# Optimization experiments

Measured on AMD Instinct MI355X. Metric: run time of the kernel, lower is better.

The kernel has to match this reference:

```python
import jax, jax.numpy as jnp
import numpy as np

NEG_INF = -1000000000.0
INPUT_SIZE = 1024
HIDDEN_SIZE = 64
B, S = 8, 2048


def setup_inputs() -> dict:
    key = jax.random.key(0)
    ks = jax.random.split(key, 8)
    scale = 1.0 / np.sqrt(INPUT_SIZE)
    inp = {
        "input": jax.random.normal(ks[0], (B, S, INPUT_SIZE), dtype=jnp.float32),
        "mask": jax.random.randint(ks[1], (B, S, S), 0, 2, dtype=jnp.int32),
        "W_q": jax.random.uniform(ks[2], (HIDDEN_SIZE, INPUT_SIZE), jnp.float32, -scale, scale),
        "b_q": jax.random.uniform(ks[3], (HIDDEN_SIZE,), jnp.float32, -scale, scale),
        "W_k": jax.random.uniform(ks[4], (HIDDEN_SIZE, INPUT_SIZE), jnp.float32, -scale, scale),
        "b_k": jax.random.uniform(ks[5], (HIDDEN_SIZE,), jnp.float32, -scale, scale),
        "W_v": jax.random.uniform(ks[6], (HIDDEN_SIZE, INPUT_SIZE), jnp.float32, -scale, scale),
        "b_v": jax.random.uniform(ks[7], (HIDDEN_SIZE,), jnp.float32, -scale, scale),
    }
    return inp


def reference(input, mask, W_q, b_q, W_k, b_k, W_v, b_v):
    inv_sqrt_d = 1.0 / np.sqrt(HIDDEN_SIZE)
    # Q/K/V projections: torch Linear is x @ W.T + b
    q = jnp.einsum('bsi,hi->bsh', input, W_q) + b_q  # (B,S,H)
    k = jnp.einsum('bsi,hi->bsh', input, W_k) + b_k
    v = jnp.einsum('bsi,hi->bsh', input, W_v) + b_v
    scores = jnp.einsum('bqh,bkh->bqk', q, k) * inv_sqrt_d  # (B,S,S)
    scores = jnp.where(mask == 0, NEG_INF, scores)
    probs = jax.nn.softmax(scores, axis=-1)
    return jnp.einsum('bqk,bkh->bqh', probs, v)  # (B,S,H)
```

## Files before the change

### kernel.cpp

```cpp
#include <hip/hip_runtime.h>

typedef __bf16 bf16;
typedef bf16 bf16x4 __attribute__((ext_vector_type(4)));
typedef bf16 bf16x8 __attribute__((ext_vector_type(8)));
typedef float floatx4 __attribute__((ext_vector_type(4)));
typedef unsigned int u32;

#define B_ 8
#define S_ 2048
#define I_ 1024
#define H_ 64
#define NEG_INF_ -1000000000.0f

__device__ __forceinline__ void async_cp16(bf16* lds_base, const bf16* g_base, int lane) {
    __builtin_amdgcn_global_load_lds(
        (const __attribute__((address_space(1))) u32*)(g_base + lane * 8),
        (__attribute__((address_space(3))) u32*)lds_base, 16, 0, 0);
}

__global__ void conv_w(const float* __restrict__ Wq, const float* __restrict__ bq,
                       const float* __restrict__ Wk, const float* __restrict__ bk,
                       const float* __restrict__ Wv, const float* __restrict__ bv,
                       bf16* __restrict__ Wc2, float* __restrict__ bc) {
    int idx = blockIdx.x * 256 + threadIdx.x;
    int n = idx >> 10, i = idx & 1023;
    float v;
    if (n < 64)       v = Wq[n * I_ + i] * 0.125f;
    else if (n < 128) v = Wk[(n - 64) * I_ + i];
    else              v = Wv[(n - 128) * I_ + i];
    int s = i >> 7, kl = i & 127;
    Wc2[(size_t)s * 26112 + n * 136 + kl] = (bf16)v;
    if (idx < 192) {
        float bb = (idx < 64) ? bq[idx] * 0.125f
                 : (idx < 128) ? bk[idx - 64] : bv[idx - 128];
        bc[idx] = bb;
    }
}

__global__ __launch_bounds__(256, 2) void qkv_gemm(const float* __restrict__ X,
                                                   const bf16* __restrict__ Wc2,
                                                   const float* __restrict__ bc,
                                                   bf16* __restrict__ Qd,
                                                   bf16* __restrict__ Kd2,
                                                   bf16* __restrict__ Vt2) {
    __shared__ __align__(16) bf16 Xs[32 * 136];
    __shared__ __align__(16) bf16 Ws[26112];

    int tid = threadIdx.x;
    int w = tid >> 6, lane = tid & 63;
    int n = lane & 15, g = lane >> 4;
    int m0 = blockIdx.x * 32;
    int mt = w & 1, nh = (w >> 1) * 96;

    floatx4 zero4 = {0.0f, 0.0f, 0.0f, 0.0f};
    floatx4 acc[6];
#pragma unroll
    for (int t = 0; t < 6; ++t) acc[t] = zero4;

    int xrow = tid >> 3, xcb = (tid & 7) * 16;
    const float* xsrc = X + (size_t)(m0 + xrow) * I_ + xcb;
    bf16* xdst = Xs + xrow * 136 + xcb;

    for (int s = 0; s < 8; ++s) {
        const float* xp = xsrc + s * 128;
        float4 x0 = *(const float4*)(xp);
        float4 x1 = *(const float4*)(xp + 4);
        float4 x2 = *(const float4*)(xp + 8);
        float4 x3 = *(const float4*)(xp + 12);
#pragma unroll
        for (int i = 0; i < 13; ++i) {
            int inst = i * 4 + w;
            if (inst < 51)
                async_cp16(Ws + inst * 512, Wc2 + (size_t)s * 26112 + inst * 512, lane);
        }
        bf16x8 b0, b1;
        b0[0] = (bf16)x0.x; b0[1] = (bf16)x0.y; b0[2] = (bf16)x0.z; b0[3] = (bf16)x0.w;
        b0[4] = (bf16)x1.x; b0[5] = (bf16)x1.y; b0[6] = (bf16)x1.z; b0[7] = (bf16)x1.w;
        b1[0] = (bf16)x2.x; b1[1] = (bf16)x2.y; b1[2] = (bf16)x2.z; b1[3] = (bf16)x2.w;
        b1[4] = (bf16)x3.x; b1[5] = (bf16)x3.y; b1[6] = (bf16)x3.z; b1[7] = (bf16)x3.w;
        *(bf16x8*)xdst = b0;
        *(bf16x8*)(xdst + 8) = b1;
        __syncthreads();

#pragma unroll
        for (int ks = 0; ks < 4; ++ks) {
            bf16x8 xa = *(bf16x8*)(Xs + (mt * 16 + n) * 136 + ks * 32 + g * 8);
#pragma unroll
            for (int nt = 0; nt < 6; ++nt) {
                bf16x8 wb = *(bf16x8*)(Ws + (nh + nt * 16 + n) * 136 + ks * 32 + g * 8);
                acc[nt] = __builtin_amdgcn_mfma_f32_16x16x32_bf16(xa, wb, acc[nt], 0, 0, 0);
            }
        }
        __syncthreads();
    }

    int b = m0 >> 11;
    int sb = (m0 & 2047) + mt * 16 + g * 4;
#pragma unroll
    for (int nt = 0; nt < 6; ++nt) {
        int ng = nh + nt * 16 + n;
        float bias = bc[ng];
        if (ng < 64) {
#pragma unroll
            for (int r = 0; r < 4; ++r)
                Qd[(size_t)(b * S_ + sb + r) * H_ + ng] = (bf16)(acc[nt][r] + bias);
        } else if (ng < 128) {
            int hc = (ng - 64) >> 3, j = (ng - 64) & 7;
#pragma unroll
            for (int r = 0; r < 4; ++r)
                Kd2[((size_t)(b * 8 + hc) * S_ + sb + r) * 8 + j] = (bf16)(acc[nt][r] + bias);
        } else {
            int hh = ng - 128, kc = sb >> 3, jj = sb & 7;
            bf16x4 pk;
#pragma unroll
            for (int r = 0; r < 4; ++r) pk[r] = (bf16)(acc[nt][r] + bias);
            *(bf16x4*)(Vt2 + ((size_t)(b * 256 + kc) * 64 + hh) * 8 + jj) = pk;
        }
    }
}

__global__ __launch_bounds__(256, 4) void attn(const bf16* __restrict__ Qd,
                                               const bf16* __restrict__ Kd2,
                                               const bf16* __restrict__ Vt2,
                                               const int* __restrict__ mask,
                                               float* __restrict__ po,
                                               float* __restrict__ pml) {
    __shared__ __align__(16) bf16 regA[8704];
    __shared__ __align__(16) bf16 Vs[16 * 528];

    int tid = threadIdx.x;
    int w = tid >> 6, lane = tid & 63;
    int n = lane & 15, g = lane >> 4;
    int bid = blockIdx.x;
    int ksp = bid & 3;
    int qt = (bid >> 2) & 31;
    int b = bid >> 7;
    int q0 = qt * 64;

    const bf16* qptr = Qd + (size_t)(b * S_ + q0 + w * 16 + n) * H_ + g * 8;
    bf16x8 qa0 = *(const bf16x8*)qptr;
    bf16x8 qa1 = *(const bf16x8*)(qptr + 32);

    floatx4 zero4 = {0.0f, 0.0f, 0.0f, 0.0f};
    floatx4 o[4];
#pragma unroll
    for (int t = 0; t < 4; ++t) o[t] = zero4;
    float m_i[4], l_i[4];
#pragma unroll
    for (int r = 0; r < 4; ++r) { m_i[r] = -INFINITY; l_i[r] = 0.0f; }

    for (int kt = ksp * 4; kt < ksp * 4 + 4; ++kt) {
        const int* mb = mask + (size_t)(b * S_ + q0 + w * 16 + g * 4) * S_ + kt * 128 + n;
        int mreg[4][8];
#pragma unroll
        for (int r = 0; r < 4; ++r)
#pragma unroll
            for (int nt = 0; nt < 8; ++nt)
                mreg[r][nt] = mb[(size_t)r * S_ + nt * 16];
#pragma unroll
        for (int j = 0; j < 4; ++j) {
            int hc = w * 2 + (j >> 1), p = j & 1;
            async_cp16(regA + hc * 1040 + p * 512,
                       Kd2 + ((size_t)(b * 8 + hc) * S_ + kt * 128 + p * 64) * 8, lane);
        }
#pragma unroll
        for (int j = 0; j < 4; ++j) {
            int kcl = w * 4 + j;
            async_cp16(Vs + kcl * 528,
                       Vt2 + ((size_t)(b * 256 + kt * 16 + kcl) * 64) * 8, lane);
        }
        __syncthreads();

        floatx4 s[8];
#pragma unroll
        for (int nt = 0; nt < 8; ++nt) {
            floatx4 a = zero4;
            a = __builtin_amdgcn_mfma_f32_16x16x32_bf16(
                    qa0, *(const bf16x8*)(regA + g * 1040 + (nt * 16 + n) * 8), a, 0, 0, 0);
            a = __builtin_amdgcn_mfma_f32_16x16x32_bf16(
                    qa1, *(const bf16x8*)(regA + (4 + g) * 1040 + (nt * 16 + n) * 8), a, 0, 0, 0);
            s[nt] = a;
        }

#pragma unroll
        for (int r = 0; r < 4; ++r)
#pragma unroll
            for (int nt = 0; nt < 8; ++nt)
                if (mreg[r][nt] == 0) s[nt][r] = NEG_INF_;
#pragma unroll
        for (int r = 0; r < 4; ++r) {
            float tm = s[0][r];
#pragma unroll
            for (int nt = 1; nt < 8; ++nt) tm = fmaxf(tm, s[nt][r]);
#pragma unroll
            for (int off = 1; off < 16; off <<= 1) tm = fmaxf(tm, __shfl_xor(tm, off, 64));
            float mn = fmaxf(m_i[r], tm);
            float alpha = __expf(m_i[r] - mn);
            m_i[r] = mn;
            float rs = 0.0f;
#pragma unroll
            for (int nt = 0; nt < 8; ++nt) {
                float p = __expf(s[nt][r] - mn);
                s[nt][r] = p;
                rs += p;
            }
#pragma unroll
            for (int off = 1; off < 16; off <<= 1) rs += __shfl_xor(rs, off, 64);
            l_i[r] = l_i[r] * alpha + rs;
#pragma unroll
            for (int ht = 0; ht < 4; ++ht) o[ht][r] *= alpha;
        }
        __syncthreads();

#pragma unroll
        for (int r = 0; r < 4; ++r)
#pragma unroll
            for (int nt = 0; nt < 8; ++nt)
                regA[(w * 16 + g * 4 + r) * 136 + nt * 16 + n] = (bf16)s[nt][r];
        __syncthreads();

#pragma unroll
        for (int k0 = 0; k0 < 4; ++k0) {
            bf16x8 pa = *(bf16x8*)(regA + (w * 16 + n) * 136 + k0 * 32 + g * 8);
#pragma unroll
            for (int ht = 0; ht < 4; ++ht) {
                bf16x8 vb = *(bf16x8*)(Vs + (k0 * 4 + g) * 528 + (ht * 16 + n) * 8);
                o[ht] = __builtin_amdgcn_mfma_f32_16x16x32_bf16(pa, vb, o[ht], 0, 0, 0);
            }
        }
        __syncthreads();
    }

    float* pb = po + (size_t)bid * 4096;
#pragma unroll
    for (int ht = 0; ht < 4; ++ht)
#pragma unroll
        for (int r = 0; r < 4; ++r)
            pb[(w * 16 + g * 4 + r) * 64 + ht * 16 + n] = o[ht][r];
    if (n == 0) {
#pragma unroll
        for (int r = 0; r < 4; ++r) {
            pml[(size_t)bid * 128 + w * 16 + g * 4 + r] = m_i[r];
            pml[(size_t)bid * 128 + 64 + w * 16 + g * 4 + r] = l_i[r];
        }
    }
}

__global__ __launch_bounds__(256) void reduce_o(const float* __restrict__ po,
                                                const float* __restrict__ pml,
                                                float* __restrict__ out) {
    int idx = blockIdx.x * 256 + threadIdx.x;
    int h = idx & 63, q = idx >> 6;
    int b = q >> 11, qq = q & 2047;
    int qt = qq >> 6, ql = qq & 63;
    int bid0 = (b * 32 + qt) * 4;
    float mj[4], lj[4], M = -INFINITY;
#pragma unroll
    for (int j = 0; j < 4; ++j) {
        mj[j] = pml[(size_t)(bid0 + j) * 128 + ql];
        lj[j] = pml[(size_t)(bid0 + j) * 128 + 64 + ql];
        M = fmaxf(M, mj[j]);
    }
    float num = 0.0f, den = 0.0f;
#pragma unroll
    for (int j = 0; j < 4; ++j) {
        float sc = __expf(mj[j] - M);
        den += lj[j] * sc;
        num += po[(size_t)(bid0 + j) * 4096 + ql * 64 + h] * sc;
    }
    out[(size_t)q * 64 + h] = num / den;
}

extern "C" void kernel_launch(void* const* d_in, const int* in_sizes, int n_in,
                              void* d_out, int out_size, void* d_ws, size_t ws_size,
                              hipStream_t stream) {
    const float* X    = (const float*)d_in[0];
    const int*   mask = (const int*)d_in[1];
    const float* Wq   = (const float*)d_in[2];
    const float* bq   = (const float*)d_in[3];
    const float* Wk   = (const float*)d_in[4];
    const float* bk   = (const float*)d_in[5];
    const float* Wv   = (const float*)d_in[6];
    const float* bv   = (const float*)d_in[7];
    float* out = (float*)d_out;

    char* p = (char*)d_ws;
    bf16* Qd   = (bf16*)p;  p += (size_t)B_ * S_ * H_ * 2;
    bf16* Kd2  = (bf16*)p;  p += (size_t)B_ * S_ * H_ * 2;
    bf16* Vt2  = (bf16*)p;  p += (size_t)B_ * S_ * H_ * 2;
    bf16* Wc2  = (bf16*)p;  p += (size_t)8 * 26112 * 2;
    float* bc  = (float*)p; p += 1024;
    float* po  = (float*)p; p += (size_t)1024 * 4096 * 4;
    float* pml = (float*)p; p += (size_t)1024 * 128 * 4;

    conv_w<<<dim3(768), dim3(256), 0, stream>>>(Wq, bq, Wk, bk, Wv, bv, Wc2, bc);
    qkv_gemm<<<dim3(512), dim3(256), 0, stream>>>(X, Wc2, bc, Qd, Kd2, Vt2);
    attn<<<dim3(1024), dim3(256), 0, stream>>>(Qd, Kd2, Vt2, mask, po, pml);
    reduce_o<<<dim3(4096), dim3(256), 0, stream>>>(po, pml, out);
}
```

Measured before the change: 267.1 us.

## Pre-pack int32 mask into bitmask before attention kernel

Adds a streaming kernel that converts the int32 attention mask into a 1-bit-per-element packed mask, read with wide coalesced loads. The attention kernel then loads four 32-bit words per row per key tile instead of 32 scattered int loads, and tests bits to apply masking. This moves the large mask read out of the latency-sensitive attention loop. The cost is an extra kernel launch and a small workspace buffer.

```diff
diff --git a/kernel.cpp b/kernel.cpp
--- a/kernel.cpp
+++ b/kernel.cpp
@@ -16,6 +16,22 @@
     __builtin_amdgcn_global_load_lds(
         (const __attribute__((address_space(1))) u32*)(g_base + lane * 8),
         (__attribute__((address_space(3))) u32*)lds_base, 16, 0, 0);
+}
+
+__global__ __launch_bounds__(256) void pack_mask(const int* __restrict__ mask,
+                                                 u32* __restrict__ pm) {
+    int d = blockIdx.x * 256 + threadIdx.x;
+    const int4* src = (const int4*)(mask + (size_t)d * 32);
+    u32 bits = 0;
+#pragma unroll
+    for (int j = 0; j < 8; ++j) {
+        int4 v = src[j];
+        bits |= (v.x != 0 ? 1u : 0u) << (j * 4);
+        bits |= (v.y != 0 ? 1u : 0u) << (j * 4 + 1);
+        bits |= (v.z != 0 ? 1u : 0u) << (j * 4 + 2);
+        bits |= (v.w != 0 ? 1u : 0u) << (j * 4 + 3);
+    }
+    pm[d] = bits;
 }
 
 __global__ void conv_w(const float* __restrict__ Wq, const float* __restrict__ bq,
@@ -122,7 +138,7 @@
 __global__ __launch_bounds__(256, 4) void attn(const bf16* __restrict__ Qd,
                                                const bf16* __restrict__ Kd2,
                                                const bf16* __restrict__ Vt2,
-                                               const int* __restrict__ mask,
+                                               const u32* __restrict__ pm,
                                                float* __restrict__ po,
                                                float* __restrict__ pml) {
     __shared__ __align__(16) bf16 regA[8704];
@@ -149,14 +165,15 @@
 #pragma unroll
     for (int r = 0; r < 4; ++r) { m_i[r] = -INFINITY; l_i[r] = 0.0f; }
 
+    const u32* pmb = pm + (size_t)(b * S_ + q0 + w * 16 + g * 4) * 64;
+
     for (int kt = ksp * 4; kt < ksp * 4 + 4; ++kt) {
-        const int* mb = mask + (size_t)(b * S_ + q0 + w * 16 + g * 4) * S_ + kt * 128 + n;
-        int mreg[4][8];
-#pragma unroll
-        for (int r = 0; r < 4; ++r)
-#pragma unroll
-            for (int nt = 0; nt < 8; ++nt)
-                mreg[r][nt] = mb[(size_t)r * S_ + nt * 16];
+        u32 mq[4][4];
+#pragma unroll
+        for (int r = 0; r < 4; ++r) {
+            uint4 t4 = *(const uint4*)(pmb + (size_t)r * 64 + kt * 4);
+            mq[r][0] = t4.x; mq[r][1] = t4.y; mq[r][2] = t4.z; mq[r][3] = t4.w;
+        }
 #pragma unroll
         for (int j = 0; j < 4; ++j) {
             int hc = w * 2 + (j >> 1), p = j & 1;
@@ -186,7 +203,9 @@
         for (int r = 0; r < 4; ++r)
 #pragma unroll
             for (int nt = 0; nt < 8; ++nt)
-                if (mreg[r][nt] == 0) s[nt][r] = NEG_INF_;
+                if (!((mq[r][nt >> 1] >> ((nt & 1) * 16 + n)) & 1u))
+                    s[nt][r] = NEG_INF_;
+
 #pragma unroll
         for (int r = 0; r < 4; ++r) {
             float tm = s[0][r];
@@ -290,11 +309,13 @@
     bf16* Vt2  = (bf16*)p;  p += (size_t)B_ * S_ * H_ * 2;
     bf16* Wc2  = (bf16*)p;  p += (size_t)8 * 26112 * 2;
     float* bc  = (float*)p; p += 1024;
+    u32*  pmb  = (u32*)p;   p += (size_t)B_ * S_ * 64 * 4;
     float* po  = (float*)p; p += (size_t)1024 * 4096 * 4;
     float* pml = (float*)p; p += (size_t)1024 * 128 * 4;
 
+    pack_mask<<<dim3(4096), dim3(256), 0, stream>>>(mask, pmb);
     conv_w<<<dim3(768), dim3(256), 0, stream>>>(Wq, bq, Wk, bk, Wv, bv, Wc2, bc);
     qkv_gemm<<<dim3(512), dim3(256), 0, stream>>>(X, Wc2, bc, Qd, Kd2, Vt2);
-    attn<<<dim3(1024), dim3(256), 0, stream>>>(Qd, Kd2, Vt2, mask, po, pml);
+    attn<<<dim3(1024), dim3(256), 0, stream>>>(Qd, Kd2, Vt2, pmb, po, pml);
     reduce_o<<<dim3(4096), dim3(256), 0, stream>>>(po, pml, out);
 }
```

Result: slower. 288.8 us (+8.1%).
